# Kernel optimization log

Measured on AMD Instinct MI355X. Metric: run time of the kernel, lower is better.

## Reference

```python
import jax, jax.numpy as jnp
import numpy as np

B, N, D_IN, D_OUT = 4, 2048, 1024, 1024


def setup_inputs() -> dict:
    key = jax.random.key(0)
    kx, kq, kk, kv = jax.random.split(key, 4)
    x = jax.random.normal(kx, (B, N, D_IN), dtype=jnp.float32)
    # torch Linear(d_in, d_out, bias=False): y = x @ W.T, W ~ U(-1/sqrt(d_in), 1/sqrt(d_in)).
    # Store as [d_in, d_out] so y = x @ W.
    bound = 1.0 / np.sqrt(D_IN)
    Wq = jax.random.uniform(kq, (D_IN, D_OUT), jnp.float32, -bound, bound)
    Wk = jax.random.uniform(kk, (D_IN, D_OUT), jnp.float32, -bound, bound)
    Wv = jax.random.uniform(kv, (D_IN, D_OUT), jnp.float32, -bound, bound)
    return {"x": x, "Wq": Wq, "Wk": Wk, "Wv": Wv}


def reference(x, Wq, Wk, Wv):
    # x: [B, N, d_in]
    q = jnp.einsum("bnd,de->bne", x, Wq)  # [B, N, d_out]
    k = jnp.einsum("bnd,de->bne", x, Wk)
    v = jnp.einsum("bnd,de->bne", x, Wv)
    n = x.shape[1]
    scores = jnp.einsum("bqe,bke->bqk", q, k)  # [B, N, N]
    causal = jnp.triu(jnp.ones((n, n), dtype=bool), k=1)  # True above diagonal -> masked
    scores = jnp.where(causal, -jnp.inf, scores)
    scale = 1.0 / jnp.sqrt(jnp.asarray(k.shape[-1], dtype=scores.dtype))
    weights = jax.nn.softmax(scores * scale, axis=-1)
    # dropout with drop_rate=0.0 is identity
    return jnp.einsum("bqk,bke->bqe", weights, v)  # [B, N, d_out]
```

## Files before the change

kernel.cpp:

```cpp
#include <hip/hip_runtime.h>

typedef float  f4v  __attribute__((ext_vector_type(4)));
typedef short  s8v  __attribute__((ext_vector_type(8)));

__device__ __forceinline__ ushort f2b(float f) {
    union { float f; unsigned int u; } v; v.f = f;
    unsigned int u = v.u;
    u += 0x7fffu + ((u >> 16) & 1u);
    return (ushort)(u >> 16);
}
__device__ __forceinline__ float b2f(ushort u) {
    union { unsigned int u; float f; } v; v.u = ((unsigned int)u) << 16;
    return v.f;
}

__device__ __forceinline__ void async16(const ushort* g, ushort* ldsp) {
    __builtin_amdgcn_global_load_lds(
        (const __attribute__((address_space(1))) unsigned int*)g,
        (__attribute__((address_space(3))) unsigned int*)ldsp, 16, 0, 0);
}

__global__ __launch_bounds__(256) void cast_f32_bf16(const float* __restrict__ in,
                                                     ushort* __restrict__ out,
                                                     float* __restrict__ l, int n4) {
    int i = blockIdx.x * 256 + threadIdx.x;
    if (i < 8192) l[i] = 0.f;
    if (i < n4) {
        float4 f = ((const float4*)in)[i];
        ushort4 o;
        o.x = f2b(f.x); o.y = f2b(f.y); o.z = f2b(f.z); o.w = f2b(f.w);
        ((ushort4*)out)[i] = o;
    }
}

__global__ __launch_bounds__(256) void transpose_cast(const float* __restrict__ w0,
                                                      const float* __restrict__ w1,
                                                      const float* __restrict__ w2,
                                                      ushort* __restrict__ out) {
    __shared__ float tile[32][33];
    const float* W = (blockIdx.z == 0) ? w0 : (blockIdx.z == 1 ? w1 : w2);
    ushort* O = out + (size_t)blockIdx.z * (1024u * 1024u);
    int x0 = blockIdx.x * 32, y0 = blockIdx.y * 32;
    int tx = threadIdx.x, ty = threadIdx.y;
    for (int i = 0; i < 4; i++)
        tile[ty + i * 8][tx] = W[(size_t)(y0 + ty + i * 8) * 1024 + x0 + tx];
    __syncthreads();
    for (int i = 0; i < 4; i++)
        O[(size_t)(x0 + ty + i * 8) * 1024 + y0 + tx] = f2b(tile[tx][ty + i * 8]);
}

#define GEMM_KLOOP64_N64(ArowP_, BrowP_, strideA_, strideB_, K0_, KMAX_)              \
    for (int k0 = (K0_); k0 < (KMAX_); k0 += 64) {                                    \
        async16(ArowP_ + k0, sAw);                                                    \
        async16(ArowP_ + k0 + 16 * (strideA_), sAw + 16 * 32);                        \
        async16(ArowP_ + k0 + 32, sAw + 4096);                                        \
        async16(ArowP_ + k0 + 32 + 16 * (strideA_), sAw + 4096 + 16 * 32);            \
        async16(BrowP_ + k0, sBw);                                                    \
        async16(BrowP_ + k0 + 32, sBw + 2048);                                        \
        __syncthreads();                                                              \
        for (int s = 0; s < 2; s++) {                                                 \
            s8v af[4], bf[2];                                                         \
            for (int mi = 0; mi < 4; mi++)                                            \
                af[mi] = *(const s8v*)&sA[s * 4096 + (wm + mi * 16 + l16) * 32 + quad * 8]; \
            for (int ni = 0; ni < 2; ni++)                                            \
                bf[ni] = *(const s8v*)&sB[s * 2048 + (wn + ni * 16 + l16) * 32 + quad * 8]; \
            for (int mi = 0; mi < 4; mi++)                                            \
                for (int ni = 0; ni < 2; ni++)                                        \
                    acc[mi][ni] = __builtin_amdgcn_mfma_f32_16x16x32_bf16(            \
                        af[mi], bf[ni], acc[mi][ni], 0, 0, 0);                        \
        }                                                                             \
        __syncthreads();                                                              \
    }

#define GEMM_PREAMBLE_N64                                                             \
    const int tid = threadIdx.x;                                                      \
    const int w = tid >> 6, lane = tid & 63, quad = lane >> 4, l16 = lane & 15;       \
    const int wm = (w >> 1) * 64, wn = (w & 1) * 32;                                  \
    f4v acc[4][2];                                                                    \
    for (int mi = 0; mi < 4; mi++)                                                    \
        for (int ni = 0; ni < 2; ni++) acc[mi][ni] = 0;                               \
    ushort* sAw = &sA[(w * 32) * 32];                                                 \
    ushort* sBw = &sB[(w * 16) * 32];

__global__ __launch_bounds__(512, 2) void gemm_qkv(const ushort* __restrict__ A,
                                                   const ushort* __restrict__ Wt,
                                                   ushort* __restrict__ q,
                                                   ushort* __restrict__ k,
                                                   ushort* __restrict__ vt) {
    constexpr int K = 1024;
    extern __shared__ ushort lds[];

    const int L = blockIdx.x;
    const int xcd = L & 7, idx = L >> 3;
    const int ci = xcd >> 1, cj = xcd & 1;
    const int mo = idx >> 3, no = idx & 7;
    const int m0 = (ci * 8 + mo) * 256;
    const int n0 = (cj * 8 + no) * 192;

    const int tid = threadIdx.x;
    const int w = tid >> 6, lane = tid & 63, quad = lane >> 4, l16 = lane & 15;
    const int wm = (w >> 1) * 64, wn = (w & 1) * 96;

    ushort* a0 = lds;
    ushort* a1 = lds + 16384;
    ushort* a2 = lds + 32768;
    ushort* b0 = lds + 49152;
    ushort* b1 = lds + 61440;

    const int lr = lane >> 3;
    const int lc8 = (lane & 7) ^ lr;
    const ushort* Ab = A  + (size_t)(m0 + w * 8 + lr) * K + lc8 * 8;
    const ushort* Bb = Wt + (size_t)(n0 + w * 8 + lr) * K + lc8 * 8;
    const int dW = w * 512;

#define ISSUE_A(buf_, kk_, a_) async16(Ab + (size_t)(a_) * 64 * K + (kk_), (buf_) + (a_) * 4096 + dW)
#define ISSUE_B(buf_, kk_, c_) async16(Bb + (size_t)(c_) * 64 * K + (kk_), (buf_) + (c_) * 4096 + dW)

#define RD_A(buf_)                                                                    \
    _Pragma("unroll") for (int mi = 0; mi < 4; mi++)                                  \
    _Pragma("unroll") for (int s = 0; s < 2; s++)                                     \
        af[mi][s] = *(const s8v*)&(buf_)[(wm + mi * 16 + l16) * 64 +                  \
                                         (((s * 4 + quad) ^ (l16 & 7)) * 8)];

#define RD_B2(buf_, NI0_)                                                             \
    _Pragma("unroll") for (int j = 0; j < 2; j++)                                     \
    _Pragma("unroll") for (int s = 0; s < 2; s++)                                     \
        bf[j][s] = *(const s8v*)&(buf_)[(wn + ((NI0_) + j) * 16 + l16) * 64 +         \
                                        (((s * 4 + quad) ^ (l16 & 7)) * 8)];

#define MFMA16(NI0_)                                                                  \
    _Pragma("unroll") for (int mi = 0; mi < 4; mi++)                                  \
    _Pragma("unroll") for (int j = 0; j < 2; j++)                                     \
    _Pragma("unroll") for (int s = 0; s < 2; s++)                                     \
        acc[mi][(NI0_) + j] = __builtin_amdgcn_mfma_f32_16x16x32_bf16(                \
            af[mi][s], bf[j][s], acc[mi][(NI0_) + j], 0, 0, 0);

    f4v acc[4][6];
    #pragma unroll
    for (int mi = 0; mi < 4; mi++)
        #pragma unroll
        for (int ni = 0; ni < 6; ni++) acc[mi][ni] = 0;

    #pragma unroll
    for (int a = 0; a < 4; a++) ISSUE_A(a0, 0, a);
    #pragma unroll
    for (int c = 0; c < 3; c++) ISSUE_B(b0, 0, c);
    #pragma unroll
    for (int a = 0; a < 4; a++) ISSUE_A(a1, 64, a);
    asm volatile("s_waitcnt vmcnt(4)" ::: "memory");
    asm volatile("s_barrier" ::: "memory");

    for (int t = 0; t < 16; ++t) {
        const int kB = (t + 1) * 64;
        const int kA = (t + 2) * 64;
        s8v af[4][2], bf[2][2];

        RD_A(a0)
        RD_B2(b0, 0)
        if (t < 15) {
            ISSUE_B(b1, kB, 0);
            ISSUE_B(b1, kB, 1);
            ISSUE_B(b1, kB, 2);
        }
        asm volatile("s_barrier" ::: "memory");
        __builtin_amdgcn_s_setprio(1);
        MFMA16(0)
        __builtin_amdgcn_s_setprio(0);
        asm volatile("s_barrier" ::: "memory");

        RD_B2(b0, 2)
        if (t < 14) {
            ISSUE_A(a2, kA, 0);
            ISSUE_A(a2, kA, 1);
        }
        asm volatile("s_barrier" ::: "memory");
        __builtin_amdgcn_s_setprio(1);
        MFMA16(2)
        __builtin_amdgcn_s_setprio(0);
        asm volatile("s_barrier" ::: "memory");

        RD_B2(b0, 4)
        if (t < 14) {
            ISSUE_A(a2, kA, 2);
            ISSUE_A(a2, kA, 3);
        }
        asm volatile("s_barrier" ::: "memory");
        __builtin_amdgcn_s_setprio(1);
        MFMA16(4)
        __builtin_amdgcn_s_setprio(0);

        if (t < 14)       asm volatile("s_waitcnt vmcnt(4)" ::: "memory");
        else if (t == 14) asm volatile("s_waitcnt vmcnt(0)" ::: "memory");
        asm volatile("s_barrier" ::: "memory");

        ushort* ta = a0; a0 = a1; a1 = a2; a2 = ta;
        ushort* tb = b0; b0 = b1; b1 = tb;
    }

    #pragma unroll
    for (int mi = 0; mi < 4; mi++)
        #pragma unroll
        for (int ni = 0; ni < 6; ni++) {
            int row = m0 + wm + mi * 16 + quad * 4;
            int col = n0 + wn + ni * 16 + l16;
            int z = col >> 10, cz = col & 1023;
            f4v v = acc[mi][ni];
            if (z < 2) {
                ushort* C = (z == 0) ? q : k;
                #pragma unroll
                for (int rr = 0; rr < 4; rr++)
                    C[(size_t)(row + rr) * 1024 + cz] = f2b(v[rr]);
            } else {
                int b = row >> 11, tok = row & 2047;
                ushort4 pk;
                pk.x = f2b(v[0]); pk.y = f2b(v[1]); pk.z = f2b(v[2]); pk.w = f2b(v[3]);
                *(ushort4*)&vt[(size_t)b * (1024u * 2048u) + (size_t)cz * 2048 + tok] = pk;
            }
        }
#undef ISSUE_A
#undef ISSUE_B
#undef RD_A
#undef RD_B2
#undef MFMA16
}

__global__ __launch_bounds__(256) void sgemm_qk(const ushort* __restrict__ Q,
                                                const ushort* __restrict__ Km,
                                                ushort* __restrict__ E,
                                                float* __restrict__ l) {
    constexpr int K = 1024;
    __shared__ ushort sA[2 * 4096];
    __shared__ ushort sB[2 * 2048];
    const int L = blockIdx.x;
    const int t = (L & 7) * 136 + (L >> 3);
    const int b = t / 272;
    const int tt = t - b * 272;
    int mt = 0;
    while ((mt + 1) * (mt + 2) <= tt) mt++;
    const int nt = tt - mt * (mt + 1);
    const ushort* A  = Q  + (size_t)b * 2048 * 1024;
    const ushort* Bt = Km + (size_t)b * 2048 * 1024;
    ushort* C = E + (size_t)b * 2048 * 2048;
    float* lb = l + (size_t)b * 2048;
    const int m0 = mt * 128, n0 = nt * 64;
    GEMM_PREAMBLE_N64
    const ushort* ArowP = A + (size_t)(m0 + w * 32 + (lane >> 2)) * K + (lane & 3) * 8;
    const ushort* BrowP = Bt + (size_t)(n0 + w * 16 + (lane >> 2)) * K + (lane & 3) * 8;
    GEMM_KLOOP64_N64(ArowP, BrowP, K, K, 0, K)

    for (int mi = 0; mi < 4; mi++) {
        for (int rr = 0; rr < 4; rr++) {
            const int row = m0 + wm + mi * 16 + quad * 4 + rr;
            float s = 0.f;
            for (int ni = 0; ni < 2; ni++) {
                int col = n0 + wn + ni * 16 + l16;
                float e = (col <= row) ? __expf(acc[mi][ni][rr] * 0.03125f) : 0.f;
                ushort eb = f2b(e);
                C[(size_t)row * 2048 + col] = eb;
                s += b2f(eb);
            }
            s += __shfl_xor(s, 1);
            s += __shfl_xor(s, 2);
            s += __shfl_xor(s, 4);
            s += __shfl_xor(s, 8);
            if (l16 == 0) atomicAdd(&lb[row], s);
        }
    }
}

__global__ __launch_bounds__(256) void gemm_pv(const ushort* __restrict__ Em,
                                               const ushort* __restrict__ Vt,
                                               const float* __restrict__ l,
                                               float* __restrict__ Out) {
    __shared__ ushort sA[2 * 4096];
    __shared__ ushort sB[2 * 2048];
    const int L = blockIdx.x;
    const int t = (L & 7) * 128 + (L >> 3);
    const int b = t >> 8;
    const int r = t & 255;
    const int qq = r >> 4;
    const int nt = r & 15;
    const int mt = (qq & 1) ? (qq >> 1) : (15 - (qq >> 1));
    const ushort* A  = Em + (size_t)b * 2048 * 2048;
    const ushort* Bt = Vt + (size_t)b * 1024 * 2048;
    const float* lb = l + (size_t)b * 2048;
    float* C = Out + (size_t)b * 2048 * 1024;
    const int m0 = mt * 128, n0 = nt * 64;
    const int Kmax = m0 + 128;
    GEMM_PREAMBLE_N64
    const ushort* ArowP = A + (size_t)(m0 + w * 32 + (lane >> 2)) * 2048 + (lane & 3) * 8;
    const ushort* BrowP = Bt + (size_t)(n0 + w * 16 + (lane >> 2)) * 2048 + (lane & 3) * 8;
    GEMM_KLOOP64_N64(ArowP, BrowP, 2048, 2048, 0, Kmax)

    for (int mi = 0; mi < 4; mi++) {
        const int row = m0 + wm + mi * 16 + quad * 4;
        float inv[4];
        for (int rr = 0; rr < 4; rr++) inv[rr] = 1.f / lb[row + rr];
        for (int ni = 0; ni < 2; ni++) {
            int col = n0 + wn + ni * 16 + l16;
            f4v v = acc[mi][ni];
            for (int rr = 0; rr < 4; rr++)
                C[(size_t)(row + rr) * 1024 + col] = v[rr] * inv[rr];
        }
    }
}

extern "C" void kernel_launch(void* const* d_in, const int* in_sizes, int n_in,
                              void* d_out, int out_size, void* d_ws, size_t ws_size,
                              hipStream_t stream) {
    const float* x  = (const float*)d_in[0];
    const float* Wq = (const float*)d_in[1];
    const float* Wk = (const float*)d_in[2];
    const float* Wv = (const float*)d_in[3];
    float* out = (float*)d_out;

    static bool init = false;
    if (!init) {
        hipFuncSetAttribute(reinterpret_cast<const void*>(gemm_qkv),
                            hipFuncAttributeMaxDynamicSharedMemorySize, 147456);
        init = true;
    }

    char* ws = (char*)d_ws;
    const size_t MiB = 1u << 20;
    ushort* xb = (ushort*)(ws);
    ushort* wt = (ushort*)(ws + 16 * MiB);
    ushort* q  = (ushort*)(ws + 22 * MiB);
    ushort* k  = (ushort*)(ws + 38 * MiB);
    ushort* vt = (ushort*)(ws + 54 * MiB);
    ushort* E  = (ushort*)(ws + 70 * MiB);
    float*  l  = (float*)(ws + 102 * MiB);

    cast_f32_bf16<<<(8192 * 1024 / 4) / 256, 256, 0, stream>>>(x, xb, l, 8192 * 1024 / 4);
    transpose_cast<<<dim3(32, 32, 3), dim3(32, 8), 0, stream>>>(Wq, Wk, Wv, wt);

    gemm_qkv<<<512, 512, 147456, stream>>>(xb, wt, q, k, vt);
    sgemm_qk<<<1088, 256, 0, stream>>>(q, k, E, l);
    gemm_pv<<<1024, 256, 0, stream>>>(E, vt, l, out);
}
```

Measured before the change: 222.5 us.

## Port QK and PV GEMMs to large-tile triple-buffered pipelined MFMA kernels

Measured after the change: 213.5 us. 1.04x faster.

```diff
diff --git a/kernel.cpp b/kernel.cpp
--- a/kernel.cpp
+++ b/kernel.cpp
@@ -49,38 +49,25 @@
         O[(size_t)(x0 + ty + i * 8) * 1024 + y0 + tx] = f2b(tile[tx][ty + i * 8]);
 }
 
-#define GEMM_KLOOP64_N64(ArowP_, BrowP_, strideA_, strideB_, K0_, KMAX_)              \
-    for (int k0 = (K0_); k0 < (KMAX_); k0 += 64) {                                    \
-        async16(ArowP_ + k0, sAw);                                                    \
-        async16(ArowP_ + k0 + 16 * (strideA_), sAw + 16 * 32);                        \
-        async16(ArowP_ + k0 + 32, sAw + 4096);                                        \
-        async16(ArowP_ + k0 + 32 + 16 * (strideA_), sAw + 4096 + 16 * 32);            \
-        async16(BrowP_ + k0, sBw);                                                    \
-        async16(BrowP_ + k0 + 32, sBw + 2048);                                        \
-        __syncthreads();                                                              \
-        for (int s = 0; s < 2; s++) {                                                 \
-            s8v af[4], bf[2];                                                         \
-            for (int mi = 0; mi < 4; mi++)                                            \
-                af[mi] = *(const s8v*)&sA[s * 4096 + (wm + mi * 16 + l16) * 32 + quad * 8]; \
-            for (int ni = 0; ni < 2; ni++)                                            \
-                bf[ni] = *(const s8v*)&sB[s * 2048 + (wn + ni * 16 + l16) * 32 + quad * 8]; \
-            for (int mi = 0; mi < 4; mi++)                                            \
-                for (int ni = 0; ni < 2; ni++)                                        \
-                    acc[mi][ni] = __builtin_amdgcn_mfma_f32_16x16x32_bf16(            \
-                        af[mi], bf[ni], acc[mi][ni], 0, 0, 0);                        \
-        }                                                                             \
-        __syncthreads();                                                              \
-    }
-
-#define GEMM_PREAMBLE_N64                                                             \
-    const int tid = threadIdx.x;                                                      \
-    const int w = tid >> 6, lane = tid & 63, quad = lane >> 4, l16 = lane & 15;       \
-    const int wm = (w >> 1) * 64, wn = (w & 1) * 32;                                  \
-    f4v acc[4][2];                                                                    \
-    for (int mi = 0; mi < 4; mi++)                                                    \
-        for (int ni = 0; ni < 2; ni++) acc[mi][ni] = 0;                               \
-    ushort* sAw = &sA[(w * 32) * 32];                                                 \
-    ushort* sBw = &sB[(w * 16) * 32];
+
+#define RD_A4(buf_)                                                                   \
+    _Pragma("unroll") for (int mi = 0; mi < 4; mi++)                                  \
+    _Pragma("unroll") for (int s = 0; s < 2; s++)                                     \
+        af[mi][s] = *(const s8v*)&(buf_)[(wm + mi * 16 + l16) * 64 +                  \
+                                         (((s * 4 + quad) ^ (l16 & 7)) * 8)];
+
+#define RD_B2(buf_, NI0_)                                                             \
+    _Pragma("unroll") for (int j = 0; j < 2; j++)                                     \
+    _Pragma("unroll") for (int s = 0; s < 2; s++)                                     \
+        bf[j][s] = *(const s8v*)&(buf_)[(wn + ((NI0_) + j) * 16 + l16) * 64 +         \
+                                        (((s * 4 + quad) ^ (l16 & 7)) * 8)];
+
+#define MFMA16(NI0_)                                                                  \
+    _Pragma("unroll") for (int mi = 0; mi < 4; mi++)                                  \
+    _Pragma("unroll") for (int j = 0; j < 2; j++)                                     \
+    _Pragma("unroll") for (int s = 0; s < 2; s++)                                     \
+        acc[mi][(NI0_) + j] = __builtin_amdgcn_mfma_f32_16x16x32_bf16(                \
+            af[mi][s], bf[j][s], acc[mi][(NI0_) + j], 0, 0, 0);
 
 __global__ __launch_bounds__(512, 2) void gemm_qkv(const ushort* __restrict__ A,
                                                    const ushort* __restrict__ Wt,
@@ -116,25 +103,6 @@
 #define ISSUE_A(buf_, kk_, a_) async16(Ab + (size_t)(a_) * 64 * K + (kk_), (buf_) + (a_) * 4096 + dW)
 #define ISSUE_B(buf_, kk_, c_) async16(Bb + (size_t)(c_) * 64 * K + (kk_), (buf_) + (c_) * 4096 + dW)
 
-#define RD_A(buf_)                                                                    \
-    _Pragma("unroll") for (int mi = 0; mi < 4; mi++)                                  \
-    _Pragma("unroll") for (int s = 0; s < 2; s++)                                     \
-        af[mi][s] = *(const s8v*)&(buf_)[(wm + mi * 16 + l16) * 64 +                  \
-                                         (((s * 4 + quad) ^ (l16 & 7)) * 8)];
-
-#define RD_B2(buf_, NI0_)                                                             \
-    _Pragma("unroll") for (int j = 0; j < 2; j++)                                     \
-    _Pragma("unroll") for (int s = 0; s < 2; s++)                                     \
-        bf[j][s] = *(const s8v*)&(buf_)[(wn + ((NI0_) + j) * 16 + l16) * 64 +         \
-                                        (((s * 4 + quad) ^ (l16 & 7)) * 8)];
-
-#define MFMA16(NI0_)                                                                  \
-    _Pragma("unroll") for (int mi = 0; mi < 4; mi++)                                  \
-    _Pragma("unroll") for (int j = 0; j < 2; j++)                                     \
-    _Pragma("unroll") for (int s = 0; s < 2; s++)                                     \
-        acc[mi][(NI0_) + j] = __builtin_amdgcn_mfma_f32_16x16x32_bf16(                \
-            af[mi][s], bf[j][s], acc[mi][(NI0_) + j], 0, 0, 0);
-
     f4v acc[4][6];
     #pragma unroll
     for (int mi = 0; mi < 4; mi++)
@@ -155,7 +123,7 @@
         const int kA = (t + 2) * 64;
         s8v af[4][2], bf[2][2];
 
-        RD_A(a0)
+        RD_A4(a0)
         RD_B2(b0, 0)
         if (t < 15) {
             ISSUE_B(b1, kB, 0);
@@ -219,90 +187,254 @@
         }
 #undef ISSUE_A
 #undef ISSUE_B
-#undef RD_A
-#undef RD_B2
-#undef MFMA16
-}
-
-__global__ __launch_bounds__(256) void sgemm_qk(const ushort* __restrict__ Q,
-                                                const ushort* __restrict__ Km,
-                                                ushort* __restrict__ E,
-                                                float* __restrict__ l) {
+}
+
+__global__ __launch_bounds__(512, 2) void sgemm_qk(const ushort* __restrict__ Q,
+                                                   const ushort* __restrict__ Km,
+                                                   ushort* __restrict__ E,
+                                                   float* __restrict__ l) {
     constexpr int K = 1024;
-    __shared__ ushort sA[2 * 4096];
-    __shared__ ushort sB[2 * 2048];
+    extern __shared__ ushort lds[];
+
     const int L = blockIdx.x;
-    const int t = (L & 7) * 136 + (L >> 3);
-    const int b = t / 272;
-    const int tt = t - b * 272;
+    const int xcd = L & 7, i = L >> 3;
+    const int t = (xcd < 4) ? (xcd * 26 + i) : (104 + (xcd - 4) * 25 + i);
+    const int b = t / 51;
+    int tt = t - b * 51;
     int mt = 0;
-    while ((mt + 1) * (mt + 2) <= tt) mt++;
-    const int nt = tt - mt * (mt + 1);
+    for (;; mt++) {
+        int c = (4 * (mt + 1) + 2) / 3;
+        if (tt < c) break;
+        tt -= c;
+    }
+    const int nt = tt;
+    const int m0 = mt * 256, n0 = nt * 192;
     const ushort* A  = Q  + (size_t)b * 2048 * 1024;
     const ushort* Bt = Km + (size_t)b * 2048 * 1024;
-    ushort* C = E + (size_t)b * 2048 * 2048;
+    ushort* Cb = E + (size_t)b * 2048 * 2048;
     float* lb = l + (size_t)b * 2048;
-    const int m0 = mt * 128, n0 = nt * 64;
-    GEMM_PREAMBLE_N64
-    const ushort* ArowP = A + (size_t)(m0 + w * 32 + (lane >> 2)) * K + (lane & 3) * 8;
-    const ushort* BrowP = Bt + (size_t)(n0 + w * 16 + (lane >> 2)) * K + (lane & 3) * 8;
-    GEMM_KLOOP64_N64(ArowP, BrowP, K, K, 0, K)
-
+
+    const int tid = threadIdx.x;
+    const int w = tid >> 6, lane = tid & 63, quad = lane >> 4, l16 = lane & 15;
+    const int wm = (w >> 1) * 64, wn = (w & 1) * 96;
+
+    ushort* a0 = lds;
+    ushort* a1 = lds + 16384;
+    ushort* a2 = lds + 32768;
+    ushort* b0 = lds + 49152;
+    ushort* b1 = lds + 61440;
+
+    const int lr = lane >> 3;
+    const int lc8 = (lane & 7) ^ lr;
+    const ushort* Ab = A  + (size_t)(m0 + w * 8 + lr) * K + lc8 * 8;
+    const ushort* Bb = Bt + (size_t)(n0 + w * 8 + lr) * K + lc8 * 8;
+    const int dW = w * 512;
+
+#define ISSUE_A(buf_, kk_, a_) async16(Ab + (size_t)(a_) * 64 * K + (kk_), (buf_) + (a_) * 4096 + dW)
+#define ISSUE_B(buf_, kk_, c_) async16(Bb + (size_t)(c_) * 64 * K + (kk_), (buf_) + (c_) * 4096 + dW)
+
+    f4v acc[4][6];
+    #pragma unroll
+    for (int mi = 0; mi < 4; mi++)
+        #pragma unroll
+        for (int ni = 0; ni < 6; ni++) acc[mi][ni] = 0;
+
+    #pragma unroll
+    for (int a = 0; a < 4; a++) ISSUE_A(a0, 0, a);
+    #pragma unroll
+    for (int c = 0; c < 3; c++) ISSUE_B(b0, 0, c);
+    #pragma unroll
+    for (int a = 0; a < 4; a++) ISSUE_A(a1, 64, a);
+    asm volatile("s_waitcnt vmcnt(4)" ::: "memory");
+    asm volatile("s_barrier" ::: "memory");
+
+    for (int tk = 0; tk < 16; ++tk) {
+        const int kB = (tk + 1) * 64;
+        const int kA = (tk + 2) * 64;
+        s8v af[4][2], bf[2][2];
+
+        RD_A4(a0)
+        RD_B2(b0, 0)
+        if (tk < 15) {
+            ISSUE_B(b1, kB, 0);
+            ISSUE_B(b1, kB, 1);
+            ISSUE_B(b1, kB, 2);
+        }
+        asm volatile("s_barrier" ::: "memory");
+        __builtin_amdgcn_s_setprio(1);
+        MFMA16(0)
+        __builtin_amdgcn_s_setprio(0);
+        asm volatile("s_barrier" ::: "memory");
+
+        RD_B2(b0, 2)
+        if (tk < 14) {
+            ISSUE_A(a2, kA, 0);
+            ISSUE_A(a2, kA, 1);
+        }
+        asm volatile("s_barrier" ::: "memory");
+        __builtin_amdgcn_s_setprio(1);
+        MFMA16(2)
+        __builtin_amdgcn_s_setprio(0);
+        asm volatile("s_barrier" ::: "memory");
+
+        RD_B2(b0, 4)
+        if (tk < 14) {
+            ISSUE_A(a2, kA, 2);
+            ISSUE_A(a2, kA, 3);
+        }
+        asm volatile("s_barrier" ::: "memory");
+        __builtin_amdgcn_s_setprio(1);
+        MFMA16(4)
+        __builtin_amdgcn_s_setprio(0);
+
+        if (tk < 14)       asm volatile("s_waitcnt vmcnt(4)" ::: "memory");
+        else if (tk == 14) asm volatile("s_waitcnt vmcnt(0)" ::: "memory");
+        asm volatile("s_barrier" ::: "memory");
+
+        ushort* ta = a0; a0 = a1; a1 = a2; a2 = ta;
+        ushort* tb = b0; b0 = b1; b1 = tb;
+    }
+
+    #pragma unroll
     for (int mi = 0; mi < 4; mi++) {
+        float rs[4] = {0.f, 0.f, 0.f, 0.f};
+        #pragma unroll
+        for (int ni = 0; ni < 6; ni++) {
+            const int colbase = n0 + wn + ni * 16;
+            if (colbase >= 2048) continue;
+            const int col = colbase + l16;
+            f4v v = acc[mi][ni];
+            #pragma unroll
+            for (int rr = 0; rr < 4; rr++) {
+                const int row = m0 + wm + mi * 16 + quad * 4 + rr;
+                float e = (col <= row) ? __expf(v[rr] * 0.03125f) : 0.f;
+                ushort eb = f2b(e);
+                Cb[(size_t)row * 2048 + col] = eb;
+                rs[rr] += b2f(eb);
+            }
+        }
+        #pragma unroll
         for (int rr = 0; rr < 4; rr++) {
-            const int row = m0 + wm + mi * 16 + quad * 4 + rr;
-            float s = 0.f;
-            for (int ni = 0; ni < 2; ni++) {
-                int col = n0 + wn + ni * 16 + l16;
-                float e = (col <= row) ? __expf(acc[mi][ni][rr] * 0.03125f) : 0.f;
-                ushort eb = f2b(e);
-                C[(size_t)row * 2048 + col] = eb;
-                s += b2f(eb);
-            }
+            float s = rs[rr];
             s += __shfl_xor(s, 1);
             s += __shfl_xor(s, 2);
             s += __shfl_xor(s, 4);
             s += __shfl_xor(s, 8);
-            if (l16 == 0) atomicAdd(&lb[row], s);
-        }
-    }
-}
-
-__global__ __launch_bounds__(256) void gemm_pv(const ushort* __restrict__ Em,
-                                               const ushort* __restrict__ Vt,
-                                               const float* __restrict__ l,
-                                               float* __restrict__ Out) {
-    __shared__ ushort sA[2 * 4096];
-    __shared__ ushort sB[2 * 2048];
+            if (l16 == 0)
+                atomicAdd(&lb[m0 + wm + mi * 16 + quad * 4 + rr], s);
+        }
+    }
+#undef ISSUE_A
+#undef ISSUE_B
+}
+
+__global__ __launch_bounds__(512, 2) void gemm_pv(const ushort* __restrict__ Em,
+                                                  const ushort* __restrict__ Vt,
+                                                  const float* __restrict__ l,
+                                                  float* __restrict__ Out) {
+    extern __shared__ ushort lds[];
     const int L = blockIdx.x;
-    const int t = (L & 7) * 128 + (L >> 3);
-    const int b = t >> 8;
-    const int r = t & 255;
-    const int qq = r >> 4;
-    const int nt = r & 15;
-    const int mt = (qq & 1) ? (qq >> 1) : (15 - (qq >> 1));
+    const int t = (L & 7) * 32 + (L >> 3);
+    const int b = t >> 6;
+    const int mt = (t >> 3) & 7;
+    const int nt = t & 7;
+    const int m0 = mt * 256, n0 = nt * 128;
+    const int NT = 4 * (mt + 1);
     const ushort* A  = Em + (size_t)b * 2048 * 2048;
     const ushort* Bt = Vt + (size_t)b * 1024 * 2048;
     const float* lb = l + (size_t)b * 2048;
     float* C = Out + (size_t)b * 2048 * 1024;
-    const int m0 = mt * 128, n0 = nt * 64;
-    const int Kmax = m0 + 128;
-    GEMM_PREAMBLE_N64
-    const ushort* ArowP = A + (size_t)(m0 + w * 32 + (lane >> 2)) * 2048 + (lane & 3) * 8;
-    const ushort* BrowP = Bt + (size_t)(n0 + w * 16 + (lane >> 2)) * 2048 + (lane & 3) * 8;
-    GEMM_KLOOP64_N64(ArowP, BrowP, 2048, 2048, 0, Kmax)
-
+
+    const int tid = threadIdx.x;
+    const int w = tid >> 6, lane = tid & 63, quad = lane >> 4, l16 = lane & 15;
+    const int wm = (w >> 1) * 64, wn = (w & 1) * 64;
+
+    ushort* a0 = lds;
+    ushort* a1 = lds + 16384;
+    ushort* a2 = lds + 32768;
+    ushort* b0 = lds + 49152;
+    ushort* b1 = lds + 57344;
+
+    const int lr = lane >> 3;
+    const int lc8 = (lane & 7) ^ lr;
+    const ushort* Ab = A  + (size_t)(m0 + w * 8 + lr) * 2048 + lc8 * 8;
+    const ushort* Bb = Bt + (size_t)(n0 + w * 8 + lr) * 2048 + lc8 * 8;
+    const int dW = w * 512;
+
+#define ISSUE_A(buf_, kk_, a_) async16(Ab + (size_t)(a_) * 64 * 2048 + (kk_), (buf_) + (a_) * 4096 + dW)
+#define ISSUE_B(buf_, kk_, c_) async16(Bb + (size_t)(c_) * 64 * 2048 + (kk_), (buf_) + (c_) * 4096 + dW)
+
+    f4v acc[4][4];
+    #pragma unroll
+    for (int mi = 0; mi < 4; mi++)
+        #pragma unroll
+        for (int ni = 0; ni < 4; ni++) acc[mi][ni] = 0;
+
+    #pragma unroll
+    for (int a = 0; a < 4; a++) ISSUE_A(a0, 0, a);
+    #pragma unroll
+    for (int c = 0; c < 2; c++) ISSUE_B(b0, 0, c);
+    #pragma unroll
+    for (int a = 0; a < 4; a++) ISSUE_A(a1, 64, a);
+    asm volatile("s_waitcnt vmcnt(4)" ::: "memory");
+    asm volatile("s_barrier" ::: "memory");
+
+    for (int tk = 0; tk < NT; ++tk) {
+        const int kB = (tk + 1) * 64;
+        const int kA = (tk + 2) * 64;
+        s8v af[4][2], bf[2][2];
+
+        RD_A4(a0)
+        RD_B2(b0, 0)
+        if (tk < NT - 1) {
+            ISSUE_B(b1, kB, 0);
+            ISSUE_B(b1, kB, 1);
+        }
+        if (tk < NT - 2) {
+            ISSUE_A(a2, kA, 0);
+            ISSUE_A(a2, kA, 1);
+        }
+        asm volatile("s_barrier" ::: "memory");
+        __builtin_amdgcn_s_setprio(1);
+        MFMA16(0)
+        __builtin_amdgcn_s_setprio(0);
+        asm volatile("s_barrier" ::: "memory");
+
+        RD_B2(b0, 2)
+        if (tk < NT - 2) {
+            ISSUE_A(a2, kA, 2);
+            ISSUE_A(a2, kA, 3);
+        }
+        asm volatile("s_barrier" ::: "memory");
+        __builtin_amdgcn_s_setprio(1);
+        MFMA16(2)
+        __builtin_amdgcn_s_setprio(0);
+
+        if (tk < NT - 2)       asm volatile("s_waitcnt vmcnt(4)" ::: "memory");
+        else if (tk == NT - 2) asm volatile("s_waitcnt vmcnt(0)" ::: "memory");
+        asm volatile("s_barrier" ::: "memory");
+
+        ushort* ta = a0; a0 = a1; a1 = a2; a2 = ta;
+        ushort* tb = b0; b0 = b1; b1 = tb;
+    }
+
+    #pragma unroll
     for (int mi = 0; mi < 4; mi++) {
         const int row = m0 + wm + mi * 16 + quad * 4;
         float inv[4];
+        #pragma unroll
         for (int rr = 0; rr < 4; rr++) inv[rr] = 1.f / lb[row + rr];
-        for (int ni = 0; ni < 2; ni++) {
-            int col = n0 + wn + ni * 16 + l16;
+        #pragma unroll
+        for (int ni = 0; ni < 4; ni++) {
+            const int col = n0 + wn + ni * 16 + l16;
             f4v v = acc[mi][ni];
+            #pragma unroll
             for (int rr = 0; rr < 4; rr++)
                 C[(size_t)(row + rr) * 1024 + col] = v[rr] * inv[rr];
         }
     }
+#undef ISSUE_A
+#undef ISSUE_B
 }
 
 extern "C" void kernel_launch(void* const* d_in, const int* in_sizes, int n_in,
@@ -318,6 +450,10 @@
     if (!init) {
         hipFuncSetAttribute(reinterpret_cast<const void*>(gemm_qkv),
                             hipFuncAttributeMaxDynamicSharedMemorySize, 147456);
+        hipFuncSetAttribute(reinterpret_cast<const void*>(sgemm_qk),
+                            hipFuncAttributeMaxDynamicSharedMemorySize, 147456);
+        hipFuncSetAttribute(reinterpret_cast<const void*>(gemm_pv),
+                            hipFuncAttributeMaxDynamicSharedMemorySize, 131072);
         init = true;
     }
 
@@ -335,6 +471,6 @@
     transpose_cast<<<dim3(32, 32, 3), dim3(32, 8), 0, stream>>>(Wq, Wk, Wv, wt);
 
     gemm_qkv<<<512, 512, 147456, stream>>>(xb, wt, q, k, vt);
-    sgemm_qk<<<1088, 256, 0, stream>>>(q, k, E, l);
-    gemm_pv<<<1024, 256, 0, stream>>>(E, vt, l, out);
-}
+    sgemm_qk<<<204, 512, 147456, stream>>>(q, k, E, l);
+    gemm_pv<<<256, 512, 131072, stream>>>(E, vt, l, out);
+}
```
